# Performance work log

Hardware: AMD Instinct MI355X
Metric: run time of the kernel (lower is better)

Reference implementation:

```python
import jax, jax.numpy as jnp
import numpy as np

B, C, HEADS, DH = 2, 1280, 20, 64
INNER = HEADS * DH
HW = 64
S = HW * HW
L = 77
ENC = 4096
GROUPS = 32
EPS = 1e-5
CREG = 1.0     # creg_ in __init__
NOATTN = 1.0   # global noattn
NORES = 1.0    # global noresidual


def setup_inputs() -> dict:
    key = jax.random.key(0)
    ks = jax.random.split(key, 10)
    std = 0.02
    return {
        "x": jax.random.normal(ks[0], (B, C, HW, HW), jnp.float32),
        "text": jax.random.normal(ks[1], (B, L, ENC), jnp.float32),
        "gn_gamma": jnp.ones((C,), jnp.float32),
        "gn_beta": jnp.zeros((C,), jnp.float32),
        "ln_gamma": jnp.ones((ENC,), jnp.float32),
        "ln_beta": jnp.zeros((ENC,), jnp.float32),
        "Wq": jax.random.normal(ks[2], (C, INNER), jnp.float32) * std,
        "bq": jnp.zeros((INNER,), jnp.float32),
        "Wk": jax.random.normal(ks[3], (ENC, INNER), jnp.float32) * std,
        "bk": jnp.zeros((INNER,), jnp.float32),
        "Wv": jax.random.normal(ks[4], (ENC, INNER), jnp.float32) * std,
        "bv": jnp.zeros((INNER,), jnp.float32),
        "Wo": jax.random.normal(ks[5], (INNER, C), jnp.float32) * std,
        "bo": jnp.zeros((C,), jnp.float32),
        "size_reg": jax.random.uniform(ks[6], (1, S, L), jnp.float32),
        "treg": jax.random.uniform(ks[7], (1,), jnp.float32),
        "mask": jax.random.randint(ks[8], (1, S, L), 0, 2, jnp.int32),
    }


def _group_norm(h, gamma, beta):
    # h: [B, C, S]; GroupNorm over (C//GROUPS, S) per group
    hg = h.reshape(B, GROUPS, -1)
    mu = hg.mean(-1, keepdims=True)
    var = hg.var(-1, keepdims=True)
    hn = ((hg - mu) * jax.lax.rsqrt(var + EPS)).reshape(B, C, S)
    return hn * gamma[None, :, None] + beta[None, :, None]


def _layer_norm(t, gamma, beta):
    mu = t.mean(-1, keepdims=True)
    var = t.var(-1, keepdims=True)
    return (t - mu) * jax.lax.rsqrt(var + EPS) * gamma + beta


def reference(x, text, gn_gamma, gn_beta, ln_gamma, ln_beta, Wq, bq, Wk, bk,
              Wv, bv, Wo, bo, size_reg, treg, mask):
    residual = x                              # [B, C, HW, HW]
    h = x.reshape(B, C, S)                    # spatial tokens
    h = _group_norm(h, gn_gamma, gn_beta).transpose(0, 2, 1)   # [B, S, C]
    enc = _layer_norm(text, ln_gamma, ln_beta)                  # [B, L, ENC]

    # head_to_batch_dim (out_dim=3): [B, T, inner] -> [B*heads, T, dh]
    q = (h @ Wq + bq).reshape(B, S, HEADS, DH).transpose(0, 2, 1, 3).reshape(B * HEADS, S, DH)
    k = (enc @ Wk + bk).reshape(B, L, HEADS, DH).transpose(0, 2, 1, 3).reshape(B * HEADS, L, DH)
    v = (enc @ Wv + bv).reshape(B, L, HEADS, DH).transpose(0, 2, 1, 3).reshape(B * HEADS, L, DH)

    scale = DH ** -0.5
    sim = jnp.einsum('bsd,bld->bsl', q, k) * scale            # [B*H, S, L]

    # region regularization applied only to the conditional (second) half
    half = (B * HEADS) // 2
    sim_u, sim_c = sim[:half], sim[half:]
    mn = sim_c.min(-1, keepdims=True)
    mx = sim_c.max(-1, keepdims=True)
    m = mask > 0                                               # [1, S, L] broadcasts over heads
    w = size_reg * CREG * treg[0]
    sim_c = sim_c + jnp.where(m, w, 0.0) * (mx - sim_c) - jnp.where(m, 0.0, w) * (sim_c - mn)
    sim = jnp.concatenate([sim_u, sim_c], axis=0)

    probs = jax.nn.softmax(sim, axis=-1)
    out = jnp.einsum('bsl,bld->bsd', probs, v)                 # [B*H, S, DH]
    # batch_to_head_dim: [B*H, S, DH] -> [B, S, inner]
    out = out.reshape(B, HEADS, S, DH).transpose(0, 2, 1, 3).reshape(B, S, INNER)
    out = out @ Wo + bo                                        # to_out[0]; dropout p=0
    out = out.transpose(0, 2, 1).reshape(residual.shape)       # [B, C, HW, HW]
    return out * NOATTN + residual * NORES
```

## Files before the change

### kernel.cpp

```cpp
#include <hip/hip_runtime.h>

typedef __bf16 bf16_t;
typedef __bf16 bf16x8 __attribute__((ext_vector_type(8)));
typedef float  f32x4  __attribute__((ext_vector_type(4)));
typedef unsigned int u32x4 __attribute__((ext_vector_type(4)));


__global__ __launch_bounds__(256) void k_transpose_cvt4(
    const float* __restrict__ w0, const float* __restrict__ w1,
    const float* __restrict__ w2, const float* __restrict__ w3,
    bf16_t* __restrict__ o0, bf16_t* __restrict__ o1,
    bf16_t* __restrict__ o2, bf16_t* __restrict__ o3)
{
  const int z = blockIdx.z;
  const float* in  = (z == 0) ? w0 : (z == 1) ? w1 : (z == 2) ? w2 : w3;
  bf16_t*      out = (z == 0) ? o0 : (z == 1) ? o1 : (z == 2) ? o2 : o3;
  const int R = (z < 2) ? 1280 : 4096;
  const int r0 = blockIdx.y * 64;
  if (r0 >= R) return;
  __shared__ float tile[64][33];
  const int c0 = blockIdx.x * 32;
  const int t = threadIdx.x;
#pragma unroll
  for (int it = 0; it < 8; ++it) {
    int r = it * 8 + (t >> 5), c = t & 31;
    tile[r][c] = in[(size_t)(r0 + r) * 1280 + c0 + c];
  }
  __syncthreads();
  {
    const int oc  = t >> 3;
    const int seg = t & 7;
    bf16x8 o;
#pragma unroll
    for (int e = 0; e < 8; ++e) o[e] = (bf16_t)tile[seg * 8 + e][oc];
    *(bf16x8*)(out + (size_t)(c0 + oc) * R + r0 + seg * 8) = o;
  }
}

__global__ __launch_bounds__(256) void k_gn_partial(
    const float* __restrict__ x, float* __restrict__ partial)
{
  const int bg    = blockIdx.x >> 5;
  const int chunk = blockIdx.x & 31;
  const float* p  = x + (size_t)bg * 163840 + (size_t)chunk * 5120;
  float s1 = 0.f, s2 = 0.f;
#pragma unroll
  for (int it = 0; it < 5; ++it) {
    float4 v = *(const float4*)(p + (size_t)(it * 256 + threadIdx.x) * 4);
    s1 += v.x + v.y + v.z + v.w;
    s2 += v.x * v.x + v.y * v.y + v.z * v.z + v.w * v.w;
  }
#pragma unroll
  for (int off = 32; off > 0; off >>= 1) {
    s1 += __shfl_down(s1, off);
    s2 += __shfl_down(s2, off);
  }
  __shared__ float r1[4], r2[4];
  if ((threadIdx.x & 63) == 0) { r1[threadIdx.x >> 6] = s1; r2[threadIdx.x >> 6] = s2; }
  __syncthreads();
  if (threadIdx.x == 0) {
    partial[blockIdx.x * 2]     = r1[0] + r1[1] + r1[2] + r1[3];
    partial[blockIdx.x * 2 + 1] = r2[0] + r2[1] + r2[2] + r2[3];
  }
}

__global__ __launch_bounds__(64) void k_gn_finalize(
    const float* __restrict__ partial, float* __restrict__ stats)
{
  const int bg = threadIdx.x;
  float t1 = 0.f, t2 = 0.f;
#pragma unroll
  for (int c = 0; c < 32; ++c) {
    t1 += partial[(bg * 32 + c) * 2];
    t2 += partial[(bg * 32 + c) * 2 + 1];
  }
  const float invN = 1.0f / 163840.0f;
  float mu  = t1 * invN;
  float var = t2 * invN - mu * mu;
  stats[bg * 2]     = mu;
  stats[bg * 2 + 1] = rsqrtf(var + 1e-5f);
}

__global__ __launch_bounds__(256) void k_gn_apply(
    const float* __restrict__ x, const float* __restrict__ stats,
    const float* __restrict__ gamma, const float* __restrict__ beta,
    bf16_t* __restrict__ h)
{
  __shared__ float tile[64][65];
  const int s0 = blockIdx.x * 64;
  const int c0 = blockIdx.y * 64;
  const int b  = blockIdx.z;
  const int t  = threadIdx.x;
#pragma unroll
  for (int it = 0; it < 16; ++it) {
    int cl = it * 4 + (t >> 6);
    int sl = t & 63;
    tile[cl][sl] = x[((size_t)(b * 1280 + c0 + cl) << 12) + s0 + sl];
  }
  __syncthreads();
#pragma unroll
  for (int it = 0; it < 2; ++it) {
    int i  = it * 256 + t;
    int sl = i >> 3;
    int cg = i & 7;
    bf16x8 o;
#pragma unroll
    for (int e = 0; e < 8; ++e) {
      int c  = c0 + cg * 8 + e;
      int g  = c / 40;
      float mu = stats[(b * 32 + g) * 2];
      float rs = stats[(b * 32 + g) * 2 + 1];
      o[e] = (bf16_t)((tile[cg * 8 + e][sl] - mu) * rs * gamma[c] + beta[c]);
    }
    *(bf16x8*)(h + (size_t)(b * 4096 + s0 + sl) * 1280 + c0 + cg * 8) = o;
  }
}

__global__ __launch_bounds__(256) void k_ln(
    const float* __restrict__ text, const float* __restrict__ g,
    const float* __restrict__ bta, bf16_t* __restrict__ enc)
{
  const int row = blockIdx.x;
  const float* p = text + (size_t)row * 4096;
  float s1 = 0.f, s2 = 0.f;
  for (int i = threadIdx.x; i < 1024; i += 256) {
    float4 v = *(const float4*)(p + (size_t)i * 4);
    s1 += v.x + v.y + v.z + v.w;
    s2 += v.x * v.x + v.y * v.y + v.z * v.z + v.w * v.w;
  }
#pragma unroll
  for (int off = 32; off > 0; off >>= 1) {
    s1 += __shfl_down(s1, off);
    s2 += __shfl_down(s2, off);
  }
  __shared__ float r1[4], r2[4], sh[2];
  if ((threadIdx.x & 63) == 0) { r1[threadIdx.x >> 6] = s1; r2[threadIdx.x >> 6] = s2; }
  __syncthreads();
  if (threadIdx.x == 0) {
    float t1 = r1[0] + r1[1] + r1[2] + r1[3];
    float t2 = r2[0] + r2[1] + r2[2] + r2[3];
    const float invN = 1.0f / 4096.0f;
    float mu  = t1 * invN;
    float var = t2 * invN - mu * mu;
    sh[0] = mu;
    sh[1] = rsqrtf(var + 1e-5f);
  }
  __syncthreads();
  const float mu = sh[0], rs = sh[1];
  for (int i = threadIdx.x; i < 1024; i += 256) {
    float4 v  = *(const float4*)(p + (size_t)i * 4);
    float4 gg = *(const float4*)(g + (size_t)i * 4);
    float4 bb = *(const float4*)(bta + (size_t)i * 4);
    bf16_t* o = enc + (size_t)row * 4096 + (size_t)i * 4;
    o[0] = (bf16_t)((v.x - mu) * rs * gg.x + bb.x);
    o[1] = (bf16_t)((v.y - mu) * rs * gg.y + bb.y);
    o[2] = (bf16_t)((v.z - mu) * rs * gg.z + bb.z);
    o[3] = (bf16_t)((v.w - mu) * rs * gg.w + bb.w);
  }
}

template <int EPI>
__global__ __launch_bounds__(256, 2) void k_gemm(
    const bf16_t* __restrict__ A, const bf16_t* __restrict__ BT,
    const float* __restrict__ bias, bf16_t* __restrict__ outb,
    const float* __restrict__ xres, float* __restrict__ dout,
    int lda, int klen, int nnt)
{
  __shared__ alignas(16) bf16_t smem[36864];
  const int tid  = threadIdx.x;
  const int lane = tid & 63;
  const int wv   = tid >> 6;
  const int wm   = wv >> 1, wn = wv & 1;

  const int cpx  = gridDim.x >> 3;
  const int nbid = (blockIdx.x & 7) * cpx + (blockIdx.x >> 3);
  const int mt   = nbid / nnt, ntile = nbid % nnt;
  const int m0   = mt * 128;
  const int n0   = ntile * 64;

  f32x4 acc[4][2];
  const f32x4 fz = {0.f, 0.f, 0.f, 0.f};
#pragma unroll
  for (int i = 0; i < 4; ++i)
#pragma unroll
    for (int j = 0; j < 2; ++j) acc[i][j] = fz;

  auto stage = [&](int slot, int kt) {
    bf16_t* sA = smem + slot * 8192;
    bf16_t* sB = smem + 24576 + slot * 4096;
#pragma unroll
    for (int it = 0; it < 4; ++it) {
      int s = it * 256 + tid;
      int row = s >> 3, ch = s & 7;
      const bf16_t* ga = A + (size_t)(m0 + row) * lda + kt + ((ch ^ (row & 7)) << 3);
      __builtin_amdgcn_global_load_lds(
          (const __attribute__((address_space(1))) void*)ga,
          (__attribute__((address_space(3))) void*)((char*)sA + s * 16),
          16, 0, 0);
    }
#pragma unroll
    for (int it = 0; it < 2; ++it) {
      int s = it * 256 + tid;
      int row = s >> 3, ch = s & 7;
      const bf16_t* gb = BT + (size_t)(n0 + row) * lda + kt + ((ch ^ (row & 7)) << 3);
      __builtin_amdgcn_global_load_lds(
          (const __attribute__((address_space(1))) void*)gb,
          (__attribute__((address_space(3))) void*)((char*)sB + s * 16),
          16, 0, 0);
    }
  };

  const int nt_k = klen >> 6;
  stage(0, 0);
  stage(1, 64);

  int cur = 0, stg = 2;
  for (int t = 0; t < nt_k; ++t) {
    if (t + 1 < nt_k) { asm volatile("s_waitcnt vmcnt(6)" ::: "memory"); }
    else              { asm volatile("s_waitcnt vmcnt(0)" ::: "memory"); }
    __builtin_amdgcn_s_barrier();
    if (t + 2 < nt_k) {
      stage(stg, (t + 2) * 64);
      stg = (stg == 2) ? 0 : stg + 1;
    }
    const char* pA = (const char*)(smem + cur * 8192);
    const char* pB = (const char*)(smem + 24576 + cur * 4096);
#pragma unroll
    for (int ks = 0; ks < 2; ++ks) {
      const int kb = ks * 64 + ((lane >> 4) << 4);
      bf16x8 af[4], bfg[2];
#pragma unroll
      for (int i = 0; i < 4; ++i) {
        int r = wm * 64 + i * 16 + (lane & 15);
        af[i] = *(const bf16x8*)(pA + r * 128 + (kb ^ ((r & 7) << 4)));
      }
#pragma unroll
      for (int j = 0; j < 2; ++j) {
        int c = wn * 32 + j * 16 + (lane & 15);
        bfg[j] = *(const bf16x8*)(pB + c * 128 + (kb ^ ((c & 7) << 4)));
      }
#pragma unroll
      for (int i = 0; i < 4; ++i)
#pragma unroll
        for (int j = 0; j < 2; ++j)
          acc[i][j] = __builtin_amdgcn_mfma_f32_16x16x32_bf16(af[i], bfg[j], acc[i][j], 0, 0, 0);
    }
    cur = (cur == 2) ? 0 : cur + 1;
  }
  __syncthreads();

  if (EPI == 0) {
    bf16_t* cst = smem;
#pragma unroll
    for (int j = 0; j < 2; ++j) {
      const int n  = n0 + wn * 32 + j * 16 + (lane & 15);
      const float bs = bias[n];
      const int cl = wn * 32 + j * 16 + (lane & 15);
#pragma unroll
      for (int i = 0; i < 4; ++i) {
        const int rl = wm * 64 + i * 16 + ((lane >> 4) << 2);
#pragma unroll
        for (int r = 0; r < 4; ++r)
          cst[(rl + r) * 76 + cl] = (bf16_t)(acc[i][j][r] + bs);
      }
    }
    __syncthreads();
#pragma unroll
    for (int it = 0; it < 4; ++it) {
      int slot = it * 256 + tid;
      int row = slot >> 3, ch = slot & 7;
      u32x4 d = *(const u32x4*)(cst + row * 76 + ch * 8);
      *(u32x4*)(outb + (size_t)(m0 + row) * 1280 + n0 + ch * 8) = d;
    }
  } else {
#pragma unroll
    for (int i = 0; i < 4; ++i) {
      const int mrow = m0 + wm * 64 + i * 16 + ((lane >> 4) << 2);
#pragma unroll
      for (int j = 0; j < 2; ++j) {
        const int n = n0 + wn * 32 + j * 16 + (lane & 15);
        const int b = mrow >> 12, s = mrow & 4095;
        const size_t off = ((size_t)(b * 1280 + n) << 12) + s;
        const float bs = bias[n];
        const float4 xr = *(const float4*)(xres + off);
        float4 o;
        o.x = acc[i][j][0] + bs + xr.x;
        o.y = acc[i][j][1] + bs + xr.y;
        o.z = acc[i][j][2] + bs + xr.z;
        o.w = acc[i][j][3] + bs + xr.w;
        *(float4*)(dout + off) = o;
      }
    }
  }
}

__global__ __launch_bounds__(256, 3) void k_gemm_kv(
    const bf16_t* __restrict__ A, const bf16_t* __restrict__ BT,
    float* __restrict__ outf, int M, int lda, int klen, int nnt, int nst)
{
  __shared__ alignas(16) bf16_t smem[24576];
  const int tid  = threadIdx.x;
  const int lane = tid & 63;
  const int wv   = tid >> 6;
  const int wm   = wv >> 1, wn = wv & 1;

  const int cpx  = gridDim.x >> 3;
  const int nbid = (blockIdx.x & 7) * cpx + (blockIdx.x >> 3);
  const int mt   = nbid / nnt, ntile = nbid % nnt;
  const int m0   = mt * 128;
  const int n0   = ntile * 64;
  const int kbeg = blockIdx.z * klen;

  f32x4 acc[4][2];
  const f32x4 fz = {0.f, 0.f, 0.f, 0.f};
#pragma unroll
  for (int i = 0; i < 4; ++i)
#pragma unroll
    for (int j = 0; j < 2; ++j) acc[i][j] = fz;

  auto stage = [&](int buf, int kt) {
    bf16_t* sA = smem + buf * 8192;
    bf16_t* sB = smem + 16384 + buf * 4096;
#pragma unroll
    for (int it = 0; it < 4; ++it) {
      int slot = it * 256 + tid;
      int row  = slot >> 3, ch = slot & 7;
      int grow = m0 + row; if (grow > M - 1) grow = M - 1;
      const bf16_t* ga = A + (size_t)grow * lda + kt + ((ch ^ (row & 7)) << 3);
      __builtin_amdgcn_global_load_lds(
          (const __attribute__((address_space(1))) void*)ga,
          (__attribute__((address_space(3))) void*)((char*)sA + slot * 16),
          16, 0, 0);
    }
#pragma unroll
    for (int it = 0; it < 2; ++it) {
      int slot = it * 256 + tid;
      int row  = slot >> 3, ch = slot & 7;
      const bf16_t* gb = BT + (size_t)(n0 + row) * lda + kt + ((ch ^ (row & 7)) << 3);
      __builtin_amdgcn_global_load_lds(
          (const __attribute__((address_space(1))) void*)gb,
          (__attribute__((address_space(3))) void*)((char*)sB + slot * 16),
          16, 0, 0);
    }
  };

  const int nt_k = klen >> 6;
  stage(0, kbeg);
  if (nt_k > 1) stage(1, kbeg + 64);

  for (int t = 0; t < nt_k; ++t) {
    if (t + 1 < nt_k) { asm volatile("s_waitcnt vmcnt(6)" ::: "memory"); }
    else              { asm volatile("s_waitcnt vmcnt(0)" ::: "memory"); }
    __builtin_amdgcn_s_barrier();
    const char* pA = (const char*)(smem + (t & 1) * 8192);
    const char* pB = (const char*)(smem + 16384 + (t & 1) * 4096);
#pragma unroll
    for (int ks = 0; ks < 2; ++ks) {
      const int kb = ks * 64 + ((lane >> 4) << 4);
      bf16x8 af[4], bfg[2];
#pragma unroll
      for (int i = 0; i < 4; ++i) {
        int r = wm * 64 + i * 16 + (lane & 15);
        af[i] = *(const bf16x8*)(pA + r * 128 + (kb ^ ((r & 7) << 4)));
      }
#pragma unroll
      for (int j = 0; j < 2; ++j) {
        int c = wn * 32 + j * 16 + (lane & 15);
        bfg[j] = *(const bf16x8*)(pB + c * 128 + (kb ^ ((c & 7) << 4)));
      }
#pragma unroll
      for (int i = 0; i < 4; ++i)
#pragma unroll
        for (int j = 0; j < 2; ++j)
          acc[i][j] = __builtin_amdgcn_mfma_f32_16x16x32_bf16(af[i], bfg[j], acc[i][j], 0, 0, 0);
    }
    asm volatile("s_waitcnt lgkmcnt(0)" ::: "memory");
    __builtin_amdgcn_s_barrier();
    if (t + 2 < nt_k) stage(t & 1, kbeg + (t + 2) * 64);
  }

#pragma unroll
  for (int i = 0; i < 4; ++i) {
    const int mrow = m0 + wm * 64 + i * 16 + ((lane >> 4) << 2);
#pragma unroll
    for (int j = 0; j < 2; ++j) {
      const int n = n0 + wn * 32 + j * 16 + (lane & 15);
#pragma unroll
      for (int r = 0; r < 4; ++r)
        if (mrow + r < M)
          outf[(size_t)blockIdx.z * 154 * nst + (size_t)(mrow + r) * nst + n] = acc[i][j][r];
    }
  }
}

__global__ __launch_bounds__(256) void k_kv_reduce(
    const float* __restrict__ part, const float* __restrict__ bk,
    const float* __restrict__ bv, bf16_t* __restrict__ kb, bf16_t* __restrict__ vb)
{
  const int idx = blockIdx.x * 256 + threadIdx.x;
  if (idx >= 154 * 2560) return;
  const int r = idx / 2560, n = idx % 2560;
  float s = (n < 1280) ? bk[n] : bv[n - 1280];
#pragma unroll
  for (int sp = 0; sp < 8; ++sp) s += part[(size_t)sp * (154 * 2560) + idx];
  if (n < 1280) kb[(size_t)r * 1280 + n] = (bf16_t)s;
  else          vb[(size_t)r * 1280 + n - 1280] = (bf16_t)s;
}

__global__ __launch_bounds__(256) void k_attn(
    const bf16_t* __restrict__ q, const bf16_t* __restrict__ kbuf,
    const bf16_t* __restrict__ vbuf, bf16_t* __restrict__ ao,
    const float* __restrict__ size_reg, const int* __restrict__ mask,
    const float* __restrict__ treg)
{
  __shared__ alignas(16) bf16_t sQ[64 * 64];
  __shared__ alignas(16) bf16_t sK[80 * 64];
  __shared__ alignas(16) bf16_t sVT[64 * 104];
  __shared__ alignas(16) bf16_t sP[4 * 16 * 104];
  const int s0   = blockIdx.x * 64;
  const int bh   = blockIdx.y;
  const int b    = bh / 20, head = bh % 20;
  const int tid  = threadIdx.x, lane = tid & 63, wv = tid >> 6;
  const int ntok = lane & 15;

  const u32x4 uz = {0u, 0u, 0u, 0u};
  for (int i = tid; i < 832; i += 256) ((u32x4*)sVT)[i] = uz;
  for (int i = tid; i < 832; i += 256) ((u32x4*)sP)[i]  = uz;

  const size_t qbase = ((size_t)(b * 4096 + s0)) * 1280 + head * 64;
  for (int slot = tid; slot < 512; slot += 256) {
    int row = slot >> 3, ch = slot & 7;
    u32x4 d = *(const u32x4*)(q + qbase + (size_t)row * 1280 + ((ch ^ (row & 7)) << 3));
    *(u32x4*)((char*)sQ + slot * 16) = d;
  }
  const size_t kvbase = ((size_t)(b * 77)) * 1280 + head * 64;
  for (int slot = tid; slot < 640; slot += 256) {
    int tok = slot >> 3, ch = slot & 7;
    u32x4 d = uz;
    if (tok < 77)
      d = *(const u32x4*)(kbuf + kvbase + (size_t)tok * 1280 + ((ch ^ (tok & 7)) << 3));
    *(u32x4*)((char*)sK + slot * 16) = d;
  }
  __syncthreads();
  for (int e = tid; e < 77 * 64; e += 256) {
    int tok = e >> 6, dh = e & 63;
    sVT[dh * 104 + tok] = vbuf[kvbase + (size_t)tok * 1280 + dh];
  }
  __syncthreads();

  f32x4 sim[5];
  const f32x4 fz = {0.f, 0.f, 0.f, 0.f};
#pragma unroll
  for (int nf = 0; nf < 5; ++nf) sim[nf] = fz;
  const int qrow = wv * 16 + (lane & 15);
#pragma unroll
  for (int ks = 0; ks < 2; ++ks) {
    const int kb = ks * 64 + ((lane >> 4) << 4);
    bf16x8 aq = *(const bf16x8*)((const char*)sQ + qrow * 128 + (kb ^ ((qrow & 7) << 4)));
#pragma unroll
    for (int nf = 0; nf < 5; ++nf) {
      int tok = nf * 16 + ntok;
      bf16x8 bk = *(const bf16x8*)((const char*)sK + tok * 128 + (kb ^ ((tok & 7) << 4)));
      sim[nf] = __builtin_amdgcn_mfma_f32_16x16x32_bf16(aq, bk, sim[nf], 0, 0, 0);
    }
  }

  float vv[5][4];
#pragma unroll
  for (int nf = 0; nf < 5; ++nf)
#pragma unroll
    for (int r = 0; r < 4; ++r) vv[nf][r] = sim[nf][r] * 0.125f;

  const int rbase = s0 + wv * 16 + ((lane >> 4) << 2);

  if (b == 1) {
    const float tr = treg[0];
#pragma unroll
    for (int r = 0; r < 4; ++r) {
      float mx = -1e30f, mn = 1e30f;
#pragma unroll
      for (int nf = 0; nf < 5; ++nf)
        if (nf * 16 + ntok < 77) { mx = fmaxf(mx, vv[nf][r]); mn = fminf(mn, vv[nf][r]); }
#pragma unroll
      for (int m = 1; m < 16; m <<= 1) {
        mx = fmaxf(mx, __shfl_xor(mx, m));
        mn = fminf(mn, __shfl_xor(mn, m));
      }
      const int srow = rbase + r;
#pragma unroll
      for (int nf = 0; nf < 5; ++nf) {
        int l = nf * 16 + ntok;
        if (l < 77) {
          float w  = size_reg[srow * 77 + l] * tr;
          int   mk = mask[srow * 77 + l];
          float v  = vv[nf][r];
          vv[nf][r] = (mk > 0) ? v + w * (mx - v) : v - w * (v - mn);
        }
      }
    }
  }

#pragma unroll
  for (int r = 0; r < 4; ++r) {
    float mx = -1e30f;
#pragma unroll
    for (int nf = 0; nf < 5; ++nf)
      if (nf * 16 + ntok < 77) mx = fmaxf(mx, vv[nf][r]);
#pragma unroll
    for (int m = 1; m < 16; m <<= 1) mx = fmaxf(mx, __shfl_xor(mx, m));
    float p[5]; float sm = 0.f;
#pragma unroll
    for (int nf = 0; nf < 5; ++nf) {
      bool val = (nf * 16 + ntok) < 77;
      p[nf] = val ? __expf(vv[nf][r] - mx) : 0.f;
      sm += p[nf];
    }
#pragma unroll
    for (int m = 1; m < 16; m <<= 1) sm += __shfl_xor(sm, m);
    const float inv = 1.0f / sm;
    const int prow = ((lane >> 4) << 2) + r;
#pragma unroll
    for (int nf = 0; nf < 5; ++nf)
      sP[wv * 1664 + prow * 104 + nf * 16 + ntok] = (bf16_t)(p[nf] * inv);
  }
  __syncthreads();

  f32x4 o[4];
#pragma unroll
  for (int fd = 0; fd < 4; ++fd) o[fd] = fz;
#pragma unroll
  for (int ks = 0; ks < 3; ++ks) {
    const int kb = ks * 64 + ((lane >> 4) << 4);
    bf16x8 ap = *(const bf16x8*)((const char*)sP + wv * 3328 + (lane & 15) * 208 + kb);
#pragma unroll
    for (int fd = 0; fd < 4; ++fd) {
      bf16x8 bv = *(const bf16x8*)((const char*)sVT + (fd * 16 + (lane & 15)) * 208 + kb);
      o[fd] = __builtin_amdgcn_mfma_f32_16x16x32_bf16(ap, bv, o[fd], 0, 0, 0);
    }
  }
  const size_t obase =
      ((size_t)(b * 4096 + s0 + wv * 16 + ((lane >> 4) << 2))) * 1280 + head * 64;
#pragma unroll
  for (int fd = 0; fd < 4; ++fd)
#pragma unroll
    for (int r = 0; r < 4; ++r)
      ao[obase + (size_t)r * 1280 + fd * 16 + (lane & 15)] = (bf16_t)o[fd][r];
}

extern "C" void kernel_launch(void* const* d_in, const int* in_sizes, int n_in,
                              void* d_out, int out_size, void* d_ws, size_t ws_size,
                              hipStream_t stream)
{
  const float* x    = (const float*)d_in[0];
  const float* text = (const float*)d_in[1];
  const float* gng  = (const float*)d_in[2];
  const float* gnb  = (const float*)d_in[3];
  const float* lng  = (const float*)d_in[4];
  const float* lnb  = (const float*)d_in[5];
  const float* Wq   = (const float*)d_in[6];
  const float* bq   = (const float*)d_in[7];
  const float* Wk   = (const float*)d_in[8];
  const float* bk   = (const float*)d_in[9];
  const float* Wv   = (const float*)d_in[10];
  const float* bv   = (const float*)d_in[11];
  const float* Wo   = (const float*)d_in[12];
  const float* bo   = (const float*)d_in[13];
  const float* sreg = (const float*)d_in[14];
  const float* treg = (const float*)d_in[15];
  const int*   msk  = (const int*)d_in[16];
  float* out = (float*)d_out;

  char* ws = (char*)d_ws;
  size_t off = 0;
  auto alloc = [&](size_t bytes) {
    char* p = ws + off;
    off += (bytes + 255) & ~(size_t)255;
    return p;
  };
  float*  partial = (float*)alloc(2048 * 2 * sizeof(float));
  float*  stats   = (float*)alloc(64 * 2 * sizeof(float));
  bf16_t* WqT = (bf16_t*)alloc((size_t)1280 * 1280 * 2);
  bf16_t* WkT = (bf16_t*)alloc((size_t)1280 * 4096 * 2);
  bf16_t* WvT = (bf16_t*)alloc((size_t)1280 * 4096 * 2);
  bf16_t* WoT = (bf16_t*)alloc((size_t)1280 * 1280 * 2);
  bf16_t* h   = (bf16_t*)alloc((size_t)8192 * 1280 * 2);
  bf16_t* enc = (bf16_t*)alloc((size_t)154 * 4096 * 2);
  bf16_t* qb  = (bf16_t*)alloc((size_t)8192 * 1280 * 2);
  bf16_t* kb  = (bf16_t*)alloc((size_t)154 * 1280 * 2);
  bf16_t* vb  = (bf16_t*)alloc((size_t)154 * 1280 * 2);
  float*  part = (float*)alloc((size_t)8 * 154 * 2560 * sizeof(float));

  k_transpose_cvt4<<<dim3(40, 64, 4), 256, 0, stream>>>(Wq, Wo, Wk, Wv,
                                                        WqT, WoT, WkT, WvT);

  k_gn_partial<<<2048, 256, 0, stream>>>(x, partial);
  k_gn_finalize<<<1, 64, 0, stream>>>(partial, stats);
  k_gn_apply<<<dim3(64, 20, 2), 256, 0, stream>>>(x, stats, gng, gnb, h);
  k_ln<<<154, 256, 0, stream>>>(text, lng, lnb, enc);

  k_gemm<0><<<dim3(1280), 256, 0, stream>>>(h, WqT, bq, qb, nullptr, nullptr,
                                            1280, 1280, 20);
  k_gemm_kv<<<dim3(80, 1, 8), 256, 0, stream>>>(enc, WkT, part, 154, 4096, 512, 40, 2560);
  k_kv_reduce<<<1540, 256, 0, stream>>>(part, bk, bv, kb, vb);

  k_attn<<<dim3(64, 40), 256, 0, stream>>>(qb, kb, vb, h, sreg, msk, treg);

  k_gemm<2><<<dim3(1280), 256, 0, stream>>>(h, WoT, bo, nullptr, x, out,
                                            1280, 1280, 20);
}
```

Baseline: 177.5 us.

## Shrink GEMM K-tile to 32 with double buffering to raise occupancy

The GEMM now stages 32-wide K slices into two LDS buffers instead of 64-wide slices into three, using a new XOR swizzle for the narrower rows. This cuts shared memory per block from 72KB to 24KB and raises the launch-bounds occupancy hint from 2 to 5 blocks. In exchange there are twice as many K iterations, each with an extra barrier and an lgkmcnt wait. The epilogue still reuses the now smaller smem array (cst at stride 76 over 128 rows), which could overflow it depending on the hidden epilogue code.

```diff
diff --git a/kernel.cpp b/kernel.cpp
--- a/kernel.cpp
+++ b/kernel.cpp
@@ -160,13 +160,13 @@
 }
 
 template <int EPI>
-__global__ __launch_bounds__(256, 2) void k_gemm(
+__global__ __launch_bounds__(256, 5) void k_gemm(
     const bf16_t* __restrict__ A, const bf16_t* __restrict__ BT,
     const float* __restrict__ bias, bf16_t* __restrict__ outb,
     const float* __restrict__ xres, float* __restrict__ dout,
     int lda, int klen, int nnt)
 {
-  __shared__ alignas(16) bf16_t smem[36864];
+  __shared__ alignas(16) bf16_t smem[12288];
   const int tid  = threadIdx.x;
   const int lane = tid & 63;
   const int wv   = tid >> 6;
@@ -185,24 +185,25 @@
 #pragma unroll
     for (int j = 0; j < 2; ++j) acc[i][j] = fz;
 
-  auto stage = [&](int slot, int kt) {
-    bf16_t* sA = smem + slot * 8192;
-    bf16_t* sB = smem + 24576 + slot * 4096;
-#pragma unroll
-    for (int it = 0; it < 4; ++it) {
+  auto stage = [&](int buf, int kt) {
+    bf16_t* sA = smem + buf * 4096;
+    bf16_t* sB = smem + 8192 + buf * 2048;
+#pragma unroll
+    for (int it = 0; it < 2; ++it) {
       int s = it * 256 + tid;
-      int row = s >> 3, ch = s & 7;
-      const bf16_t* ga = A + (size_t)(m0 + row) * lda + kt + ((ch ^ (row & 7)) << 3);
+      int row = s >> 2, cs = s & 3;
+      const bf16_t* ga =
+          A + (size_t)(m0 + row) * lda + kt + ((cs ^ ((row ^ (row >> 2)) & 3)) << 3);
       __builtin_amdgcn_global_load_lds(
           (const __attribute__((address_space(1))) void*)ga,
           (__attribute__((address_space(3))) void*)((char*)sA + s * 16),
           16, 0, 0);
     }
-#pragma unroll
-    for (int it = 0; it < 2; ++it) {
-      int s = it * 256 + tid;
-      int row = s >> 3, ch = s & 7;
-      const bf16_t* gb = BT + (size_t)(n0 + row) * lda + kt + ((ch ^ (row & 7)) << 3);
+    {
+      int s = tid;
+      int row = s >> 2, cs = s & 3;
+      const bf16_t* gb =
+          BT + (size_t)(n0 + row) * lda + kt + ((cs ^ ((row ^ (row >> 2)) & 3)) << 3);
       __builtin_amdgcn_global_load_lds(
           (const __attribute__((address_space(1))) void*)gb,
           (__attribute__((address_space(3))) void*)((char*)sB + s * 16),
@@ -210,44 +211,37 @@
     }
   };
 
-  const int nt_k = klen >> 6;
+  const int nt_k = klen >> 5;
   stage(0, 0);
-  stage(1, 64);
-
-  int cur = 0, stg = 2;
+  stage(1, 32);
+
+  const int kg = lane >> 4;
   for (int t = 0; t < nt_k; ++t) {
-    if (t + 1 < nt_k) { asm volatile("s_waitcnt vmcnt(6)" ::: "memory"); }
+    if (t + 1 < nt_k) { asm volatile("s_waitcnt vmcnt(3)" ::: "memory"); }
     else              { asm volatile("s_waitcnt vmcnt(0)" ::: "memory"); }
     __builtin_amdgcn_s_barrier();
-    if (t + 2 < nt_k) {
-      stage(stg, (t + 2) * 64);
-      stg = (stg == 2) ? 0 : stg + 1;
-    }
-    const char* pA = (const char*)(smem + cur * 8192);
-    const char* pB = (const char*)(smem + 24576 + cur * 4096);
-#pragma unroll
-    for (int ks = 0; ks < 2; ++ks) {
-      const int kb = ks * 64 + ((lane >> 4) << 4);
-      bf16x8 af[4], bfg[2];
-#pragma unroll
-      for (int i = 0; i < 4; ++i) {
-        int r = wm * 64 + i * 16 + (lane & 15);
-        af[i] = *(const bf16x8*)(pA + r * 128 + (kb ^ ((r & 7) << 4)));
-      }
-#pragma unroll
-      for (int j = 0; j < 2; ++j) {
-        int c = wn * 32 + j * 16 + (lane & 15);
-        bfg[j] = *(const bf16x8*)(pB + c * 128 + (kb ^ ((c & 7) << 4)));
-      }
-#pragma unroll
-      for (int i = 0; i < 4; ++i)
-#pragma unroll
-        for (int j = 0; j < 2; ++j)
-          acc[i][j] = __builtin_amdgcn_mfma_f32_16x16x32_bf16(af[i], bfg[j], acc[i][j], 0, 0, 0);
-    }
-    cur = (cur == 2) ? 0 : cur + 1;
-  }
-  __syncthreads();
+    const char* pA = (const char*)(smem + (t & 1) * 4096);
+    const char* pB = (const char*)(smem + 8192 + (t & 1) * 2048);
+    bf16x8 af[4], bfg[2];
+#pragma unroll
+    for (int i = 0; i < 4; ++i) {
+      int r = wm * 64 + i * 16 + (lane & 15);
+      af[i] = *(const bf16x8*)(pA + r * 64 + ((kg ^ ((r ^ (r >> 2)) & 3)) << 4));
+    }
+#pragma unroll
+    for (int j = 0; j < 2; ++j) {
+      int c = wn * 32 + j * 16 + (lane & 15);
+      bfg[j] = *(const bf16x8*)(pB + c * 64 + ((kg ^ ((c ^ (c >> 2)) & 3)) << 4));
+    }
+#pragma unroll
+    for (int i = 0; i < 4; ++i)
+#pragma unroll
+      for (int j = 0; j < 2; ++j)
+        acc[i][j] = __builtin_amdgcn_mfma_f32_16x16x32_bf16(af[i], bfg[j], acc[i][j], 0, 0, 0);
+    asm volatile("s_waitcnt lgkmcnt(0)" ::: "memory");
+    __builtin_amdgcn_s_barrier();
+    if (t + 2 < nt_k) stage(t & 1, (t + 2) * 32);
+  }
 
   if (EPI == 0) {
     bf16_t* cst = smem;
```

Result: slower. 199.9 us (+12.6%).
